# Kernel optimization log

Hardware: AMD Instinct MI355X
Metric: run time of the kernel (lower is better)

## Reference

```python
import jax, jax.numpy as jnp
import numpy as np


def setup_inputs() -> dict:
    key = jax.random.key(0)
    k1, k2 = jax.random.split(key)
    B, T, F = 8, 1000, 257
    m = jax.random.normal(k1, (B, 27, T, F), dtype=jnp.float32)
    x = jax.random.normal(k2, (B, F, T, 2), dtype=jnp.float32)
    v = jnp.array([[1.0, -0.5, -0.5], [0.0, np.sqrt(3) / 2, -np.sqrt(3) / 2]], dtype=jnp.float32)
    return {"m": m, "x": x, "v": v}


def reference(m, x, v):
    B, C, T, F = m.shape
    # m -> (B, 3, 9, T, F); contract the complex-basis dim (3) with v rows
    m5 = m.reshape(B, 3, C // 3, T, F)
    H_real = jnp.einsum('k,bkntf->bntf', v[0], m5)  # (B, 9, T, F)
    H_imag = jnp.einsum('k,bkntf->bntf', v[1], m5)
    M_real = H_real.reshape(B, 3, 3, T, F)
    M_imag = H_imag.reshape(B, 3, 3, T, F)

    # x: (B,F,T,2) -> (B,2,T,F), pad: time causal (top=2), freq symmetric (1,1)
    xp = jnp.transpose(x, (0, 3, 2, 1))
    xp = jnp.pad(xp, ((0, 0), (0, 0), (2, 0), (1, 1)))
    # 3x3 unfold as 9 shifted views: (B, 2, 3, 3, T, F)
    xu = jnp.stack(
        [xp[:, :, i:i + T, j:j + F] for i in range(3) for j in range(3)],
        axis=2,
    ).reshape(B, 2, 3, 3, T, F)

    xr, xi = xu[:, 0], xu[:, 1]
    x_enh_real = jnp.sum(M_real * xr - M_imag * xi, axis=(1, 2))  # (B, T, F)
    x_enh_imag = jnp.sum(M_real * xi + M_imag * xr, axis=(1, 2))
    x_enh = jnp.stack([x_enh_real, x_enh_imag], axis=3)  # (B, T, F, 2)
    return jnp.transpose(x_enh, (0, 2, 1, 3))  # (B, F, T, 2)
```

## Files before the change

### kernel.cpp

```cpp
#include <hip/hip_runtime.h>


constexpr int B = 8, C = 27, T = 1000, F = 257;
constexpr int TCH = 4;
constexpr int NT  = T / TCH;
constexpr int GRP = 320;
constexpr int BLK = 3 * GRP;
constexpr int TROW  = TCH + 2;
constexpr int ROWSU = 259;
constexpr int RP    = 7;
constexpr int PLANE = 260 * RP;
constexpr int RPITCH = 260;

__global__ __launch_bounds__(BLK, 8)
void ccm_kernel(const float* __restrict__ m,
                const float* __restrict__ x,
                float* __restrict__ out) {
    __shared__ float xs[2 * PLANE];
    __shared__ float rs[2 * TCH * RPITCH * 2];

    const int bid = blockIdx.x;
    const int tc  = bid % NT;
    const int b   = bid / NT;
    const int t0  = tc * TCH;
    const int tx  = threadIdx.x;
    const int g   = tx / GRP;
    const int f   = tx - g * GRP;
    const bool active = (f < F);

    const float* xb = x + (size_t)b * F * T * 2;

    for (int p = tx; p < ROWSU * TROW; p += BLK) {
        const int row = p / TROW;
        const int tt  = p - row * TROW;
        const int ff  = row - 1;
        const int t   = t0 - 2 + tt;
        float re = 0.f, im = 0.f;
        if (ff >= 0 && ff < F && t >= 0) {
            const float2 v = *reinterpret_cast<const float2*>(
                xb + ((size_t)ff * T + t) * 2);
            re = v.x; im = v.y;
        }
        xs[row * RP + tt]         = re;
        xs[PLANE + row * RP + tt] = im;
    }

    const float SQ3_2 = 0.8660254037844386f;
    const float ckr = (g == 0) ? 1.0f : -0.5f;
    const float cki = (g == 0) ? 0.0f : ((g == 1) ? SQ3_2 : -SQ3_2);

    constexpr size_t CS = (size_t)T * F;
    const float* mb = m + (((size_t)b * C + 9 * g) * T + t0) * F;

    float2 res[TCH];
    float Am[9], Bm[9];

#define LOADM(DST, U)                                                     \
    {                                                                     \
        _Pragma("unroll")                                                 \
        for (int n = 0; n < 9; ++n)                                       \
            DST[n] = mb[(size_t)n * CS + (size_t)(U) * F + f];            \
    }

#define STEP(AV, U)                                                       \
    {                                                                     \
        _Pragma("unroll")                                                 \
        for (int j = 0; j < 3; ++j) {                                     \
            const float xr = xs[(f + j) * RP + ((U) + 2)];                \
            const float xi = xs[PLANE + (f + j) * RP + ((U) + 2)];        \
            wr[2][j] = ckr * xr - cki * xi;                               \
            wi[2][j] = ckr * xi + cki * xr;                               \
        }                                                                 \
        float accr = 0.f, acci = 0.f;                                     \
        _Pragma("unroll")                                                 \
        for (int i = 0; i < 3; ++i) {                                     \
            _Pragma("unroll")                                             \
            for (int j = 0; j < 3; ++j) {                                 \
                const int n = i * 3 + j;                                  \
                accr += AV[n] * wr[i][j];                                 \
                acci += AV[n] * wi[i][j];                                 \
            }                                                             \
        }                                                                 \
        res[U] = make_float2(accr, acci);                                 \
        _Pragma("unroll")                                                 \
        for (int j = 0; j < 3; ++j) {                                     \
            wr[0][j] = wr[1][j]; wi[0][j] = wi[1][j];                     \
            wr[1][j] = wr[2][j]; wi[1][j] = wi[2][j];                     \
        }                                                                 \
    }

    if (active) {
        LOADM(Am, 0);
        LOADM(Bm, 1);
    }
    __syncthreads();

    float wr[3][3], wi[3][3];
    if (active) {
        #pragma unroll
        for (int p = 0; p < 2; ++p) {
            #pragma unroll
            for (int j = 0; j < 3; ++j) {
                const float xr = xs[(f + j) * RP + p];
                const float xi = xs[PLANE + (f + j) * RP + p];
                wr[p][j] = ckr * xr - cki * xi;
                wi[p][j] = ckr * xi + cki * xr;
            }
        }

        STEP(Am, 0);  LOADM(Am, 2);
        STEP(Bm, 1);  LOADM(Bm, 3);
        STEP(Am, 2);
        STEP(Bm, 3);

        if (g > 0) {
            float2* slab = reinterpret_cast<float2*>(rs) +
                           (size_t)(g - 1) * TCH * RPITCH;
            #pragma unroll
            for (int r = 0; r < TCH; ++r)
                slab[r * RPITCH + f] = res[r];
        }
    }
#undef LOADM
#undef STEP

    __syncthreads();

    if (g == 0 && active) {
        const float2* s1 = reinterpret_cast<const float2*>(rs);
        const float2* s2 = s1 + (size_t)TCH * RPITCH;
        #pragma unroll
        for (int r = 0; r < TCH; ++r) {
            const float2 p1 = s1[r * RPITCH + f];
            const float2 p2 = s2[r * RPITCH + f];
            res[r].x += p1.x + p2.x;
            res[r].y += p1.y + p2.y;
        }
        float* op = out + ((size_t)(b * F + f) * T + t0) * 2;
        #pragma unroll
        for (int u = 0; u < TCH / 2; ++u) {
            reinterpret_cast<float4*>(op)[u] =
                make_float4(res[2 * u].x, res[2 * u].y,
                            res[2 * u + 1].x, res[2 * u + 1].y);
        }
    }
}

extern "C" void kernel_launch(void* const* d_in, const int* in_sizes, int n_in,
                              void* d_out, int out_size, void* d_ws, size_t ws_size,
                              hipStream_t stream) {
    const float* m = (const float*)d_in[0];
    const float* x = (const float*)d_in[1];
    float* out = (float*)d_out;

    const int grid = B * NT;
    ccm_kernel<<<grid, BLK, 0, stream>>>(m, x, out);
}
```

Before: 56.57 us.

## Double time chunk per block with two-phase x staging and cooperative output reduction

Each block now processes 8 time steps instead of 4. The x halo is staged into shared memory in two phases of 6 rows, and the 3x3 sliding window registers are carried across the two phases. All three groups write their partial results to shared memory, and every thread then helps reduce them and write coalesced float4 outputs spread across frequency and time-quarter. This halves the block count and the redundant halo reloads. In exchange it adds extra barriers and a larger shared-memory footprint (about 63KB), which may reduce occupancy.

New measurement: 66.14 us. 1.17x slower.

```diff
diff --git a/kernel.cpp b/kernel.cpp
--- a/kernel.cpp
+++ b/kernel.cpp
@@ -2,22 +2,22 @@
 
 
 constexpr int B = 8, C = 27, T = 1000, F = 257;
-constexpr int TCH = 4;
+constexpr int TCH = 8;
 constexpr int NT  = T / TCH;
 constexpr int GRP = 320;
 constexpr int BLK = 3 * GRP;
-constexpr int TROW  = TCH + 2;
-constexpr int ROWSU = 259;
-constexpr int RP    = 7;
+constexpr int HROW = 6;
+constexpr int RP   = 7;
 constexpr int PLANE = 260 * RP;
-constexpr int RPITCH = 260;
+constexpr int SLABP = 257;
+constexpr size_t CS = (size_t)T * F;
 
 __global__ __launch_bounds__(BLK, 8)
 void ccm_kernel(const float* __restrict__ m,
                 const float* __restrict__ x,
                 float* __restrict__ out) {
-    __shared__ float xs[2 * PLANE];
-    __shared__ float rs[2 * TCH * RPITCH * 2];
+    __shared__ float  xs[2 * PLANE];
+    __shared__ float2 rs[3 * TCH * SLABP];
 
     const int bid = blockIdx.x;
     const int tc  = bid % NT;
@@ -30,39 +30,40 @@
 
     const float* xb = x + (size_t)b * F * T * 2;
 
-    for (int p = tx; p < ROWSU * TROW; p += BLK) {
-        const int row = p / TROW;
-        const int tt  = p - row * TROW;
-        const int ff  = row - 1;
-        const int t   = t0 - 2 + tt;
-        float re = 0.f, im = 0.f;
-        if (ff >= 0 && ff < F && t >= 0) {
-            const float2 v = *reinterpret_cast<const float2*>(
-                xb + ((size_t)ff * T + t) * 2);
-            re = v.x; im = v.y;
-        }
-        xs[row * RP + tt]         = re;
-        xs[PLANE + row * RP + tt] = im;
-    }
-
     const float SQ3_2 = 0.8660254037844386f;
     const float ckr = (g == 0) ? 1.0f : -0.5f;
     const float cki = (g == 0) ? 0.0f : ((g == 1) ? SQ3_2 : -SQ3_2);
 
-    constexpr size_t CS = (size_t)T * F;
     const float* mb = m + (((size_t)b * C + 9 * g) * T + t0) * F;
 
-    float2 res[TCH];
     float Am[9], Bm[9];
+    float wr[3][3], wi[3][3];
 
-#define LOADM(DST, U)                                                     \
+    auto stage = [&](int tb) {
+        for (int p = tx; p < 259 * HROW; p += BLK) {
+            const int row = p / HROW;
+            const int tt  = p - row * HROW;
+            const int ff  = row - 1;
+            const int t   = tb + tt;
+            float re = 0.f, im = 0.f;
+            if (ff >= 0 && ff < F && t >= 0) {
+                const float2 v = *reinterpret_cast<const float2*>(
+                    xb + ((size_t)ff * T + t) * 2);
+                re = v.x; im = v.y;
+            }
+            xs[row * RP + tt]         = re;
+            xs[PLANE + row * RP + tt] = im;
+        }
+    };
+
+#define LOADM(DST, S)                                                     \
     {                                                                     \
         _Pragma("unroll")                                                 \
         for (int n = 0; n < 9; ++n)                                       \
-            DST[n] = mb[(size_t)n * CS + (size_t)(U) * F + f];            \
+            DST[n] = mb[(size_t)n * CS + (size_t)(S) * F + f];            \
     }
 
-#define STEP(AV, U)                                                       \
+#define STEP(AV, S, U)                                                    \
     {                                                                     \
         _Pragma("unroll")                                                 \
         for (int j = 0; j < 3; ++j) {                                     \
@@ -81,7 +82,7 @@
                 acci += AV[n] * wi[i][j];                                 \
             }                                                             \
         }                                                                 \
-        res[U] = make_float2(accr, acci);                                 \
+        rs[g * (TCH * SLABP) + (S) * SLABP + f] = make_float2(accr, acci);\
         _Pragma("unroll")                                                 \
         for (int j = 0; j < 3; ++j) {                                     \
             wr[0][j] = wr[1][j]; wi[0][j] = wi[1][j];                     \
@@ -93,9 +94,9 @@
         LOADM(Am, 0);
         LOADM(Bm, 1);
     }
+    stage(t0 - 2);
     __syncthreads();
 
-    float wr[3][3], wi[3][3];
     if (active) {
         #pragma unroll
         for (int p = 0; p < 2; ++p) {
@@ -107,42 +108,38 @@
                 wi[p][j] = ckr * xi + cki * xr;
             }
         }
+        STEP(Am, 0, 0);  LOADM(Am, 2);
+        STEP(Bm, 1, 1);  LOADM(Bm, 3);
+        STEP(Am, 2, 2);  LOADM(Am, 4);
+        STEP(Bm, 3, 3);  LOADM(Bm, 5);
+    }
+    __syncthreads();
 
-        STEP(Am, 0);  LOADM(Am, 2);
-        STEP(Bm, 1);  LOADM(Bm, 3);
-        STEP(Am, 2);
-        STEP(Bm, 3);
+    stage(t0 + 2);
+    __syncthreads();
 
-        if (g > 0) {
-            float2* slab = reinterpret_cast<float2*>(rs) +
-                           (size_t)(g - 1) * TCH * RPITCH;
-            #pragma unroll
-            for (int r = 0; r < TCH; ++r)
-                slab[r * RPITCH + f] = res[r];
-        }
+    if (active) {
+        STEP(Am, 4, 0);  LOADM(Am, 6);
+        STEP(Bm, 5, 1);  LOADM(Bm, 7);
+        STEP(Am, 6, 2);
+        STEP(Bm, 7, 3);
     }
 #undef LOADM
 #undef STEP
-
     __syncthreads();
 
-    if (g == 0 && active) {
-        const float2* s1 = reinterpret_cast<const float2*>(rs);
-        const float2* s2 = s1 + (size_t)TCH * RPITCH;
+    for (int task = tx; task < F * 4; task += BLK) {
+        const int ff = task >> 2;
+        const int q  = task & 3;
+        float4 o = make_float4(0.f, 0.f, 0.f, 0.f);
         #pragma unroll
-        for (int r = 0; r < TCH; ++r) {
-            const float2 p1 = s1[r * RPITCH + f];
-            const float2 p2 = s2[r * RPITCH + f];
-            res[r].x += p1.x + p2.x;
-            res[r].y += p1.y + p2.y;
+        for (int gg = 0; gg < 3; ++gg) {
+            const float2 p0 = rs[gg * (TCH * SLABP) + (2 * q) * SLABP + ff];
+            const float2 p1 = rs[gg * (TCH * SLABP) + (2 * q + 1) * SLABP + ff];
+            o.x += p0.x; o.y += p0.y; o.z += p1.x; o.w += p1.y;
         }
-        float* op = out + ((size_t)(b * F + f) * T + t0) * 2;
-        #pragma unroll
-        for (int u = 0; u < TCH / 2; ++u) {
-            reinterpret_cast<float4*>(op)[u] =
-                make_float4(res[2 * u].x, res[2 * u].y,
-                            res[2 * u + 1].x, res[2 * u + 1].y);
-        }
+        *reinterpret_cast<float4*>(
+            out + ((size_t)(b * F + ff) * T + t0) * 2 + q * 4) = o;
     }
 }
 
```
